# Performance work log

Hardware: AMD Instinct MI355X
Metric: run time of the kernel (lower is better)

Reference implementation:

```python
import jax, jax.numpy as jnp
import numpy as np

GAMMA = 0.5
LENS = 0.5
WINDOW = 10  # window_size from init

@jax.custom_vjp
def act_fun(x):
    # Heaviside forward, Gaussian surrogate backward (matches torch ActFun)
    return (x > 0).astype(x.dtype)

def _act_fwd(x):
    return act_fun(x), x

def _act_bwd(x, g):
    temp = jnp.exp(-x * x / (2 * LENS * LENS)) / (np.sqrt(2 * np.pi) * LENS)
    return (GAMMA * g * temp,)

act_fun.defvjp(_act_fwd, _act_bwd)

def mem_update(inputs, mem, thr):
    # decay_neu == 1
    mem = mem + inputs
    spike = act_fun(mem - thr)
    mem = mem * (1 - spike)
    neg = (mem < -thr).astype(mem.dtype)
    mem = mem * (1 - neg) - thr * neg
    return mem, spike

def setup_inputs() -> dict:
    key = jax.random.key(0)
    ks = jax.random.split(key, 6)
    B, T, D, H, O = 128, 100, 2048, 1024, 20
    return {
        "input": jax.random.normal(ks[0], (B, T, D), jnp.float32),
        "labels": jax.random.randint(ks[1], (B,), 0, O),
        "hidden_mem": jnp.zeros((B, H), jnp.float32),
        "hidden_spike": jnp.zeros((B, H), jnp.float32),
        "output_mem": jnp.zeros((B, O), jnp.float32),
        "output_spike": jnp.zeros((B, O), jnp.float32),
        "Wi2h": jax.random.normal(ks[2], (H, D), jnp.float32) / np.sqrt(D).astype(np.float32),
        "bi2h": jnp.zeros((H,), jnp.float32),
        "Wh2h": jax.random.normal(ks[3], (H, H), jnp.float32) / np.sqrt(H).astype(np.float32),
        "bh2h": jnp.zeros((H,), jnp.float32),
        "Wh2o": jax.random.normal(ks[4], (O, H), jnp.float32) / np.sqrt(H).astype(np.float32),
        "bh2o": jnp.zeros((O,), jnp.float32),
        "thr_h": jnp.ones((H,), jnp.float32),
        "thr_o": jnp.ones((O,), jnp.float32),
    }

def reference(input, labels, hidden_mem, hidden_spike, output_mem, output_spike,
              Wi2h, bi2h, Wh2h, bh2h, Wh2o, bh2o, thr_h, thr_o):
    B = input.shape[0]

    def step(carry, x_t):
        hm, hs, om, osp, osum = carry
        h_in = x_t @ Wi2h.T + bi2h + hs @ Wh2h.T + bh2h
        hm, hs = mem_update(h_in, hm, thr_h)
        om, osp = mem_update(hs @ Wh2o.T + bh2o, om, thr_o)
        osum = osum + osp
        nbr = (jnp.sum(osp) + jnp.sum(hs)) / B
        return (hm, hs, om, osp, osum), (hs, nbr)

    osum0 = jnp.zeros_like(output_spike)
    carry0 = (hidden_mem, hidden_spike, output_mem, output_spike, osum0)
    (hm, hs, om, osp, osum), (hs_t, nbr_events) = jax.lax.scan(
        step, carry0, jnp.swapaxes(input, 0, 1))  # scan over T

    hidden_spike_t = jnp.transpose(hs_t, (1, 2, 0))  # [B, H, T]
    # moving average over time windows (unfold + mean), stride 1
    c = jnp.cumsum(jnp.pad(hidden_spike_t, ((0, 0), (0, 0), (1, 0))), axis=2)
    hidden_spike_filt = (c[:, :, WINDOW:] - c[:, :, :-WINDOW]) / WINDOW  # [B,H,T-W+1]

    logp = jax.nn.log_softmax(osum, axis=1)
    predictions = jnp.argmax(logp, axis=1)[None, :]  # [1, B]
    loss = -jnp.mean(logp[jnp.arange(B), labels])  # NLLLoss on log_softmax
    return predictions, loss, nbr_events, hidden_spike_filt
```

## Files before the change

kernel.cpp:

```cpp
#include <hip/hip_runtime.h>
#include <hip/hip_bf16.h>
#include <cstdint>
#include <cstddef>

#define B_ 128
#define T_ 100
#define D_ 2048
#define H_ 1024
#define O_ 20

__global__ __launch_bounds__(256) void prep_kernel(const float* __restrict__ Wh2o,
                                                   float* __restrict__ W2oT,
                                                   float* __restrict__ nbr)
{
    int i = blockIdx.x * 256 + threadIdx.x;
    if (i < H_ * O_) {
        int hh = i / O_;
        int oo = i - hh * O_;
        W2oT[i] = Wh2o[oo * H_ + hh];
    }
    if (i < T_) nbr[i] = 0.0f;
}

__global__ __launch_bounds__(256) void transpose_kernel(const float* __restrict__ A,
                                                        float* __restrict__ AT)
{
    __shared__ float tile[32][33];
    int bx = blockIdx.x * 32, by = blockIdx.y * 32;
    int tx = threadIdx.x, ty = threadIdx.y;
#pragma unroll
    for (int i = 0; i < 32; i += 8)
        tile[ty + i][tx] = A[(size_t)(by + ty + i) * H_ + bx + tx];
    __syncthreads();
#pragma unroll
    for (int i = 0; i < 32; i += 8)
        AT[(size_t)(bx + ty + i) * H_ + by + tx] = tile[tx][ty + i];
}

__global__ __launch_bounds__(256) void gemm_xi_kernel(
    const float* __restrict__ X,
    const float* __restrict__ W,
    const float* __restrict__ bi2h,
    const float* __restrict__ bh2h,
    float* __restrict__ Xi)
{
    constexpr int BM = 128, BN = 128, BK = 16;
    __shared__ float As[BK][BM + 4];
    __shared__ float Bs[BK][BN + 4];
    const int tid = threadIdx.x;
    const int m0 = blockIdx.x * BM;
    const int n0 = blockIdx.y * BN;
    const int tm = tid >> 4;
    const int tn = tid & 15;
    const int ldr = tid >> 2;
    const int ldc = (tid & 3) << 2;

    float acc[8][8];
#pragma unroll
    for (int i = 0; i < 8; ++i)
#pragma unroll
        for (int j = 0; j < 8; ++j) acc[i][j] = 0.0f;

    for (int k0 = 0; k0 < D_; k0 += BK) {
#pragma unroll
        for (int p = 0; p < 2; ++p) {
            int r = ldr + p * 64;
            float4 v = *(const float4*)(X + (size_t)(m0 + r) * D_ + k0 + ldc);
            As[ldc + 0][r] = v.x; As[ldc + 1][r] = v.y;
            As[ldc + 2][r] = v.z; As[ldc + 3][r] = v.w;
        }
#pragma unroll
        for (int p = 0; p < 2; ++p) {
            int r = ldr + p * 64;
            float4 v = *(const float4*)(W + (size_t)(n0 + r) * D_ + k0 + ldc);
            Bs[ldc + 0][r] = v.x; Bs[ldc + 1][r] = v.y;
            Bs[ldc + 2][r] = v.z; Bs[ldc + 3][r] = v.w;
        }
        __syncthreads();
#pragma unroll
        for (int k = 0; k < BK; ++k) {
            float4 A0 = *(const float4*)&As[k][tm * 8];
            float4 A1 = *(const float4*)&As[k][tm * 8 + 4];
            float4 B0 = *(const float4*)&Bs[k][tn * 8];
            float4 B1 = *(const float4*)&Bs[k][tn * 8 + 4];
            float a[8] = {A0.x, A0.y, A0.z, A0.w, A1.x, A1.y, A1.z, A1.w};
            float bb[8] = {B0.x, B0.y, B0.z, B0.w, B1.x, B1.y, B1.z, B1.w};
#pragma unroll
            for (int i = 0; i < 8; ++i)
#pragma unroll
                for (int j = 0; j < 8; ++j) acc[i][j] += a[i] * bb[j];
        }
        __syncthreads();
    }

    float bsum[8];
#pragma unroll
    for (int j = 0; j < 8; ++j) {
        int n = n0 + tn * 8 + j;
        bsum[j] = bi2h[n] + bh2h[n];
    }
#pragma unroll
    for (int i = 0; i < 8; ++i) {
        size_t row = (size_t)(m0 + tm * 8 + i);
        float4 o0 = {acc[i][0] + bsum[0], acc[i][1] + bsum[1],
                     acc[i][2] + bsum[2], acc[i][3] + bsum[3]};
        float4 o1 = {acc[i][4] + bsum[4], acc[i][5] + bsum[5],
                     acc[i][6] + bsum[6], acc[i][7] + bsum[7]};
        *(float4*)(Xi + row * H_ + n0 + tn * 8)     = o0;
        *(float4*)(Xi + row * H_ + n0 + tn * 8 + 4) = o1;
    }
}

__global__ __launch_bounds__(1024) void phase2_kernel(
    const float* __restrict__ Xi,
    const float* __restrict__ WT,
    const float* __restrict__ W2oT,
    const float* __restrict__ bh2o,
    const float* __restrict__ thr_h_g,
    const float* __restrict__ thr_o_g,
    const float* __restrict__ hm0,
    const float* __restrict__ hs0,
    const float* __restrict__ om0,
    ulonglong2* __restrict__ spk,
    float* __restrict__ osum_out,
    float* __restrict__ nbr_acc)
{
    const int b = blockIdx.x;
    const int h = threadIdx.x;
    const int lane = h & 63;
    const int wv = h >> 6;

    __shared__ int   s_list[H_];
    __shared__ int   s_cnt;
    __shared__ float s_opart[16][O_];
    __shared__ int   s_wpop[16];
    __shared__ float s_om[O_];
    __shared__ float s_osum[O_];
    __shared__ float s_tho[O_];
    __shared__ float s_bo[O_];

    float hm = hm0[(size_t)b * H_ + h];
    const float thr = thr_h_g[h];

    if (h < O_) {
        s_om[h]   = om0[(size_t)b * O_ + h];
        s_osum[h] = 0.0f;
        s_tho[h]  = thr_o_g[h];
        s_bo[h]   = bh2o[h];
    }
    if (h == 0) s_cnt = 0;
    __syncthreads();
    {
        bool act = hs0[(size_t)b * H_ + h] > 0.5f;
        unsigned long long mask = __ballot(act);
        int base = 0;
        if (lane == 0) { int pc = __popcll(mask); if (pc) base = atomicAdd(&s_cnt, pc); }
        base = __shfl(base, 0);
        if (act) s_list[base + __popcll(mask & ((1ull << lane) - 1ull))] = h;
    }
    __syncthreads();

    unsigned long long bits0 = 0, bits1 = 0;
    const float* wtb = WT + h;

    for (int t = 0; t < T_; ++t) {
        float acc = Xi[((size_t)b * T_ + t) * H_ + h];
        int cnt = s_cnt;
        float a0 = 0.f, a1 = 0.f, a2 = 0.f, a3 = 0.f;
        int l = 0;
        for (; l + 4 <= cnt; l += 4) {
            int j0 = s_list[l + 0];
            int j1 = s_list[l + 1];
            int j2 = s_list[l + 2];
            int j3 = s_list[l + 3];
            a0 += wtb[(size_t)j0 << 10];
            a1 += wtb[(size_t)j1 << 10];
            a2 += wtb[(size_t)j2 << 10];
            a3 += wtb[(size_t)j3 << 10];
        }
        for (; l < cnt; ++l) a0 += wtb[(size_t)s_list[l] << 10];
        acc += (a0 + a1) + (a2 + a3);

        hm += acc;
        bool sp = (hm - thr) > 0.0f;
        if (sp) hm = 0.0f;
        if (hm < -thr) hm = -thr;
        if (sp) { if (t < 64) bits0 |= (1ull << t); else bits1 |= (1ull << (t - 64)); }

        __syncthreads();
        if (h == 0) s_cnt = 0;
        __syncthreads();
        unsigned long long mask = __ballot(sp);
        int pc = __popcll(mask);
        int base = 0;
        if (lane == 0) { s_wpop[wv] = pc; if (pc) base = atomicAdd(&s_cnt, pc); }
        base = __shfl(base, 0);
        if (sp) s_list[base + __popcll(mask & ((1ull << lane) - 1ull))] = h;
        __syncthreads();

        cnt = s_cnt;
        int per = (cnt + 15) >> 4;
        int lo = wv * per;
        int hi = lo + per; if (hi > cnt) hi = cnt;
        if (lane < O_) {
            float op = 0.0f;
            for (int q = lo; q < hi; ++q) {
                int j = s_list[q];
                op += W2oT[j * O_ + lane];
            }
            s_opart[wv][lane] = op;
        }
        __syncthreads();

        float osp_local = 0.0f;
        if (h < O_) {
            float oin = s_bo[h];
#pragma unroll
            for (int w = 0; w < 16; ++w) oin += s_opart[w][h];
            float om = s_om[h] + oin;
            float osp = ((om - s_tho[h]) > 0.0f) ? 1.0f : 0.0f;
            if (osp > 0.5f) om = 0.0f;
            if (om < -s_tho[h]) om = -s_tho[h];
            s_om[h] = om;
            s_osum[h] += osp;
            osp_local = osp;
        }
        if (h < 64) {
            float c = osp_local;
            c += __shfl_xor(c, 1);
            c += __shfl_xor(c, 2);
            c += __shfl_xor(c, 4);
            c += __shfl_xor(c, 8);
            c += __shfl_xor(c, 16);
            c += __shfl_xor(c, 32);
            if (lane == 0) {
                int hidcnt = 0;
#pragma unroll
                for (int w = 0; w < 16; ++w) hidcnt += s_wpop[w];
                atomicAdd(&nbr_acc[t], c + (float)hidcnt);
            }
        }
    }

    ulonglong2 vv; vv.x = bits0; vv.y = bits1;
    spk[(size_t)b * H_ + h] = vv;
    if (h < O_) osum_out[(size_t)b * O_ + h] = s_osum[h];
}

__global__ __launch_bounds__(256) void filt_kernel(const ulonglong2* __restrict__ spk,
                                                   float* __restrict__ outf)
{
    int i = blockIdx.x * 256 + threadIdx.x;
    ulonglong2 v = spk[i];
    float* o = outf + (size_t)i * 91;
    int s = __popcll(v.x & 0x3FFull);
    o[0] = (float)s * 0.1f;
#pragma unroll 1
    for (int tau = 1; tau <= 90; ++tau) {
        int ta = tau + 9, tsb = tau - 1;
        int add = (ta < 64) ? (int)((v.x >> ta) & 1ull) : (int)((v.y >> (ta - 64)) & 1ull);
        int sub = (tsb < 64) ? (int)((v.x >> tsb) & 1ull) : (int)((v.y >> (tsb - 64)) & 1ull);
        s += add - sub;
        o[tau] = (float)s * 0.1f;
    }
}

__global__ __launch_bounds__(256) void final_kernel(const float* __restrict__ osum,
                                                    const int* __restrict__ labels,
                                                    float* __restrict__ dout)
{
    __shared__ float s_loss[B_];
    int tid = threadIdx.x;
    if (tid < B_) {
        int b = tid;
        float v[O_];
#pragma unroll
        for (int o = 0; o < O_; ++o) v[o] = osum[b * O_ + o];
        float mv = v[0];
        int am = 0;
#pragma unroll
        for (int o = 1; o < O_; ++o)
            if (v[o] > mv) { mv = v[o]; am = o; }
        float se = 0.0f;
#pragma unroll
        for (int o = 0; o < O_; ++o) se += expf(v[o] - mv);
        float lse = mv + logf(se);
        int lab = labels[b];
        dout[b] = (float)am;
        s_loss[b] = v[lab] - lse;
    }
    if (tid >= 128 && tid < 128 + T_) {
        dout[129 + (tid - 128)] *= (1.0f / (float)B_);
    }
    __syncthreads();
    if (tid == 0) {
        float s = 0.0f;
        for (int b = 0; b < B_; ++b) s += s_loss[b];
        dout[128] = -s / (float)B_;
    }
}

extern "C" void kernel_launch(void* const* d_in, const int* in_sizes, int n_in,
                              void* d_out, int out_size, void* d_ws, size_t ws_size,
                              hipStream_t stream)
{
    const float* input  = (const float*)d_in[0];
    const int*   labels = (const int*)d_in[1];
    const float* hm0    = (const float*)d_in[2];
    const float* hs0    = (const float*)d_in[3];
    const float* om0    = (const float*)d_in[4];
    const float* Wi2h   = (const float*)d_in[6];
    const float* bi2h   = (const float*)d_in[7];
    const float* Wh2h   = (const float*)d_in[8];
    const float* bh2h   = (const float*)d_in[9];
    const float* Wh2o   = (const float*)d_in[10];
    const float* bh2o   = (const float*)d_in[11];
    const float* thr_h  = (const float*)d_in[12];
    const float* thr_o  = (const float*)d_in[13];

    float* out  = (float*)d_out;
    float* nbr  = out + 129;
    float* filt = out + 229;

    char* ws = (char*)d_ws;
    float*      Xi   = (float*)(ws);
    float*      WT   = (float*)(ws + 52428800);
    float*      W2oT = (float*)(ws + 56623104);
    ulonglong2* spk  = (ulonglong2*)(ws + 56705024);
    float*      osum = (float*)(ws + 58802176);

    prep_kernel<<<80, 256, 0, stream>>>(Wh2o, W2oT, nbr);
    transpose_kernel<<<dim3(32, 32), dim3(32, 8), 0, stream>>>(Wh2h, WT);
    gemm_xi_kernel<<<dim3(100, 8), 256, 0, stream>>>(input, Wi2h, bi2h, bh2h, Xi);
    phase2_kernel<<<128, 1024, 0, stream>>>(Xi, WT, W2oT, bh2o, thr_h, thr_o,
                                            hm0, hs0, om0, spk, osum, nbr);
    filt_kernel<<<512, 256, 0, stream>>>(spk, filt);
    final_kernel<<<1, 256, 0, stream>>>(osum, labels, out);
}
```

Measured before the change: 2.234 ms.

## Split recurrent scan across block pairs with global-flag spike exchange and float4 gathers

The per-batch recurrent kernel now runs as two 512-thread blocks, each owning half of the hidden units. The halves exchange spike masks and partial output sums every timestep through global memory with release/acquire flags. This doubles the number of blocks in flight and switches the Wh2h gather to float4 row loads split across four thread groups, reduced through shared memory. The output weights are cached in shared memory and the spike list is rebuilt from ballot masks instead of atomics. The gemm thread-to-tile mapping is also reordered. The costs are cross-block spin-wait synchronisation every step, which relies on both blocks of a pair being resident at once, plus extra barriers.

```diff
diff --git a/kernel.cpp b/kernel.cpp
--- a/kernel.cpp
+++ b/kernel.cpp
@@ -8,10 +8,16 @@
 #define D_ 2048
 #define H_ 1024
 #define O_ 20
+#define H2 512
+
+__device__ inline void f4acc(float4& a, const float4 v) {
+    a.x += v.x; a.y += v.y; a.z += v.z; a.w += v.w;
+}
 
 __global__ __launch_bounds__(256) void prep_kernel(const float* __restrict__ Wh2o,
                                                    float* __restrict__ W2oT,
-                                                   float* __restrict__ nbr)
+                                                   float* __restrict__ nbr,
+                                                   int* __restrict__ g_flag)
 {
     int i = blockIdx.x * 256 + threadIdx.x;
     if (i < H_ * O_) {
@@ -20,6 +26,7 @@
         W2oT[i] = Wh2o[oo * H_ + hh];
     }
     if (i < T_) nbr[i] = 0.0f;
+    if (i < B_ * 2) g_flag[i] = 0;
 }
 
 __global__ __launch_bounds__(256) void transpose_kernel(const float* __restrict__ A,
@@ -50,8 +57,10 @@
     const int tid = threadIdx.x;
     const int m0 = blockIdx.x * BM;
     const int n0 = blockIdx.y * BN;
-    const int tm = tid >> 4;
-    const int tn = tid & 15;
+    const int wave = tid >> 6;
+    const int lane = tid & 63;
+    const int tm = ((wave >> 1) << 3) | (lane >> 3);
+    const int tn = ((wave & 1) << 3) | (lane & 7);
     const int ldr = tid >> 2;
     const int ldc = (tid & 3) << 2;
 
@@ -111,7 +120,7 @@
     }
 }
 
-__global__ __launch_bounds__(1024) void phase2_kernel(
+__global__ __launch_bounds__(512) void phase2_kernel(
     const float* __restrict__ Xi,
     const float* __restrict__ WT,
     const float* __restrict__ W2oT,
@@ -121,130 +130,200 @@
     const float* __restrict__ hm0,
     const float* __restrict__ hs0,
     const float* __restrict__ om0,
+    unsigned long long* __restrict__ g_mask,
+    float* __restrict__ g_opart,
+    int* __restrict__ g_flag,
     ulonglong2* __restrict__ spk,
     float* __restrict__ osum_out,
     float* __restrict__ nbr_acc)
 {
-    const int b = blockIdx.x;
-    const int h = threadIdx.x;
-    const int lane = h & 63;
-    const int wv = h >> 6;
-
+    const int pair = blockIdx.x >> 1;
+    const int half = blockIdx.x & 1;
+    const int b = pair;
+    const int tid = threadIdx.x;
+    const int lane = tid & 63;
+    const int wv = tid >> 6;
+    const int h0 = half * H2;
+    const int h = h0 + tid;
+
+    __shared__ float s_W2o[H2 * O_];
     __shared__ int   s_list[H_];
+    __shared__ float4 s_red[4][128];
+    __shared__ unsigned long long s_mask[16];
+    __shared__ float s_opart[8][O_];
+    __shared__ float s_popart[O_];
+    __shared__ int   s_base[16];
     __shared__ int   s_cnt;
-    __shared__ float s_opart[16][O_];
-    __shared__ int   s_wpop[16];
-    __shared__ float s_om[O_];
-    __shared__ float s_osum[O_];
-    __shared__ float s_tho[O_];
-    __shared__ float s_bo[O_];
+    __shared__ float s_om[O_], s_osum[O_], s_tho[O_], s_bo[O_];
+
+    for (int idx = tid; idx < H2 * O_; idx += 512)
+        s_W2o[idx] = W2oT[h0 * O_ + idx];
 
     float hm = hm0[(size_t)b * H_ + h];
     const float thr = thr_h_g[h];
 
-    if (h < O_) {
-        s_om[h]   = om0[(size_t)b * O_ + h];
-        s_osum[h] = 0.0f;
-        s_tho[h]  = thr_o_g[h];
-        s_bo[h]   = bh2o[h];
-    }
-    if (h == 0) s_cnt = 0;
+    if (half == 0 && tid < O_) {
+        s_om[tid]   = om0[b * O_ + tid];
+        s_osum[tid] = 0.0f;
+        s_tho[tid]  = thr_o_g[tid];
+        s_bo[tid]   = bh2o[tid];
+    }
+
+    {
+        bool a1 = hs0[(size_t)b * H_ + wv * 64 + lane] > 0.5f;
+        bool a2 = hs0[(size_t)b * H_ + H2 + wv * 64 + lane] > 0.5f;
+        unsigned long long m1 = __ballot(a1), m2 = __ballot(a2);
+        if (lane == 0) { s_mask[wv] = m1; s_mask[8 + wv] = m2; }
+    }
+    __syncthreads();
+    if (tid == 0) {
+        int a = 0;
+#pragma unroll
+        for (int w = 0; w < 16; ++w) { s_base[w] = a; a += __popcll(s_mask[w]); }
+        s_cnt = a;
+    }
     __syncthreads();
     {
-        bool act = hs0[(size_t)b * H_ + h] > 0.5f;
-        unsigned long long mask = __ballot(act);
-        int base = 0;
-        if (lane == 0) { int pc = __popcll(mask); if (pc) base = atomicAdd(&s_cnt, pc); }
-        base = __shfl(base, 0);
-        if (act) s_list[base + __popcll(mask & ((1ull << lane) - 1ull))] = h;
+        int j = tid; int w = j >> 6; unsigned long long mw = s_mask[w];
+        if ((mw >> (j & 63)) & 1ull)
+            s_list[s_base[w] + __popcll(mw & ((1ull << (j & 63)) - 1ull))] = j;
+        j = tid + H2; w = j >> 6; mw = s_mask[w];
+        if ((mw >> (j & 63)) & 1ull)
+            s_list[s_base[w] + __popcll(mw & ((1ull << (j & 63)) - 1ull))] = j;
     }
     __syncthreads();
 
+    const float4* __restrict__ wt4 = (const float4*)WT + (h0 >> 2);
+    const int g = tid >> 7;
+    const int cid = tid & 127;
     unsigned long long bits0 = 0, bits1 = 0;
-    const float* wtb = WT + h;
 
     for (int t = 0; t < T_; ++t) {
-        float acc = Xi[((size_t)b * T_ + t) * H_ + h];
-        int cnt = s_cnt;
-        float a0 = 0.f, a1 = 0.f, a2 = 0.f, a3 = 0.f;
-        int l = 0;
-        for (; l + 4 <= cnt; l += 4) {
-            int j0 = s_list[l + 0];
-            int j1 = s_list[l + 1];
-            int j2 = s_list[l + 2];
-            int j3 = s_list[l + 3];
-            a0 += wtb[(size_t)j0 << 10];
-            a1 += wtb[(size_t)j1 << 10];
-            a2 += wtb[(size_t)j2 << 10];
-            a3 += wtb[(size_t)j3 << 10];
-        }
-        for (; l < cnt; ++l) a0 += wtb[(size_t)s_list[l] << 10];
-        acc += (a0 + a1) + (a2 + a3);
-
-        hm += acc;
+        const int cnt = s_cnt;
+        float4 a0 = {0,0,0,0}, a1 = {0,0,0,0}, a2 = {0,0,0,0}, a3 = {0,0,0,0};
+        int l = g;
+        for (; l + 12 < cnt; l += 16) {
+            int j0 = s_list[l], j1 = s_list[l + 4], j2 = s_list[l + 8], j3 = s_list[l + 12];
+            f4acc(a0, wt4[(size_t)j0 * 256 + cid]);
+            f4acc(a1, wt4[(size_t)j1 * 256 + cid]);
+            f4acc(a2, wt4[(size_t)j2 * 256 + cid]);
+            f4acc(a3, wt4[(size_t)j3 * 256 + cid]);
+        }
+        for (; l < cnt; l += 4) f4acc(a0, wt4[(size_t)s_list[l] * 256 + cid]);
+        f4acc(a0, a1); f4acc(a2, a3); f4acc(a0, a2);
+        s_red[g][cid] = a0;
+        __syncthreads();
+
+        float val = 0.0f;
+        const float* rf = (const float*)s_red;
+#pragma unroll
+        for (int gg = 0; gg < 4; ++gg) val += rf[gg * 512 + tid];
+
+        hm += Xi[((size_t)b * T_ + t) * H_ + h] + val;
         bool sp = (hm - thr) > 0.0f;
         if (sp) hm = 0.0f;
         if (hm < -thr) hm = -thr;
         if (sp) { if (t < 64) bits0 |= (1ull << t); else bits1 |= (1ull << (t - 64)); }
 
-        __syncthreads();
-        if (h == 0) s_cnt = 0;
-        __syncthreads();
-        unsigned long long mask = __ballot(sp);
-        int pc = __popcll(mask);
-        int base = 0;
-        if (lane == 0) { s_wpop[wv] = pc; if (pc) base = atomicAdd(&s_cnt, pc); }
-        base = __shfl(base, 0);
-        if (sp) s_list[base + __popcll(mask & ((1ull << lane) - 1ull))] = h;
-        __syncthreads();
-
-        cnt = s_cnt;
-        int per = (cnt + 15) >> 4;
-        int lo = wv * per;
-        int hi = lo + per; if (hi > cnt) hi = cnt;
+        unsigned long long m = __ballot(sp);
+        const int myword = half * 8 + wv;
+        if (lane == 0) s_mask[myword] = m;
+
+        float op = 0.0f;
         if (lane < O_) {
-            float op = 0.0f;
-            for (int q = lo; q < hi; ++q) {
-                int j = s_list[q];
-                op += W2oT[j * O_ + lane];
+            unsigned long long mm = m;
+            while (mm) {
+                int bit = __builtin_ctzll(mm);
+                mm &= mm - 1;
+                op += s_W2o[(wv * 64 + bit) * O_ + lane];
             }
             s_opart[wv][lane] = op;
         }
-        __syncthreads();
-
-        float osp_local = 0.0f;
-        if (h < O_) {
-            float oin = s_bo[h];
-#pragma unroll
-            for (int w = 0; w < 16; ++w) oin += s_opart[w][h];
-            float om = s_om[h] + oin;
-            float osp = ((om - s_tho[h]) > 0.0f) ? 1.0f : 0.0f;
-            if (osp > 0.5f) om = 0.0f;
-            if (om < -s_tho[h]) om = -s_tho[h];
-            s_om[h] = om;
-            s_osum[h] += osp;
-            osp_local = osp;
-        }
-        if (h < 64) {
-            float c = osp_local;
-            c += __shfl_xor(c, 1);
-            c += __shfl_xor(c, 2);
-            c += __shfl_xor(c, 4);
-            c += __shfl_xor(c, 8);
-            c += __shfl_xor(c, 16);
-            c += __shfl_xor(c, 32);
-            if (lane == 0) {
-                int hidcnt = 0;
-#pragma unroll
-                for (int w = 0; w < 16; ++w) hidcnt += s_wpop[w];
-                atomicAdd(&nbr_acc[t], c + (float)hidcnt);
+
+        const int buf = t & 1;
+        unsigned long long* gm = g_mask + (((size_t)(pair * 2 + buf) * 2 + half) * 8);
+        if (lane == 0)
+            __hip_atomic_store(&gm[wv], m, __ATOMIC_RELAXED, __HIP_MEMORY_SCOPE_AGENT);
+        __syncthreads();
+
+        float ownpart = 0.0f;
+        if (tid < O_) {
+            float s = 0.0f;
+#pragma unroll
+            for (int w = 0; w < 8; ++w) s += s_opart[w][tid];
+            ownpart = s;
+            float* go = g_opart + (((size_t)(pair * 2 + buf) * 2 + half) * O_);
+            __hip_atomic_store(&go[tid], s, __ATOMIC_RELAXED, __HIP_MEMORY_SCOPE_AGENT);
+        }
+        __syncthreads();
+        if (tid == 0) {
+            __hip_atomic_store(&g_flag[pair * 2 + half], t + 1,
+                               __ATOMIC_RELEASE, __HIP_MEMORY_SCOPE_AGENT);
+            while (__hip_atomic_load(&g_flag[pair * 2 + (half ^ 1)],
+                                     __ATOMIC_ACQUIRE, __HIP_MEMORY_SCOPE_AGENT) < t + 1)
+                __builtin_amdgcn_s_sleep(1);
+        }
+        __syncthreads();
+
+        const unsigned long long* pm =
+            g_mask + (((size_t)(pair * 2 + buf) * 2 + (half ^ 1)) * 8);
+        if (tid < 8)
+            s_mask[(half ^ 1) * 8 + tid] =
+                __hip_atomic_load(&pm[tid], __ATOMIC_RELAXED, __HIP_MEMORY_SCOPE_AGENT);
+        if (half == 0 && tid < O_) {
+            const float* po = g_opart + (((size_t)(pair * 2 + buf) * 2 + 1) * O_);
+            s_popart[tid] =
+                __hip_atomic_load(&po[tid], __ATOMIC_RELAXED, __HIP_MEMORY_SCOPE_AGENT);
+        }
+        __syncthreads();
+
+        if (half == 0) {
+            float osp_l = 0.0f;
+            if (tid < O_) {
+                float oin = s_bo[tid] + ownpart + s_popart[tid];
+                float om = s_om[tid] + oin;
+                float osp = ((om - s_tho[tid]) > 0.0f) ? 1.0f : 0.0f;
+                if (osp > 0.5f) om = 0.0f;
+                if (om < -s_tho[tid]) om = -s_tho[tid];
+                s_om[tid] = om;
+                s_osum[tid] += osp;
+                osp_l = osp;
             }
-        }
+            if (wv == 0) {
+                float c = osp_l;
+                c += __shfl_xor(c, 1);  c += __shfl_xor(c, 2);
+                c += __shfl_xor(c, 4);  c += __shfl_xor(c, 8);
+                c += __shfl_xor(c, 16); c += __shfl_xor(c, 32);
+                if (lane == 0) {
+                    int hc = 0;
+#pragma unroll
+                    for (int w = 0; w < 16; ++w) hc += __popcll(s_mask[w]);
+                    atomicAdd(&nbr_acc[t], c + (float)hc);
+                }
+            }
+        }
+
+        if (tid == 0) {
+            int a = 0;
+#pragma unroll
+            for (int w = 0; w < 16; ++w) { s_base[w] = a; a += __popcll(s_mask[w]); }
+            s_cnt = a;
+        }
+        __syncthreads();
+        {
+            int j = tid; int w = j >> 6; unsigned long long mw = s_mask[w];
+            if ((mw >> (j & 63)) & 1ull)
+                s_list[s_base[w] + __popcll(mw & ((1ull << (j & 63)) - 1ull))] = j;
+            j = tid + H2; w = j >> 6; mw = s_mask[w];
+            if ((mw >> (j & 63)) & 1ull)
+                s_list[s_base[w] + __popcll(mw & ((1ull << (j & 63)) - 1ull))] = j;
+        }
+        __syncthreads();
     }
 
     ulonglong2 vv; vv.x = bits0; vv.y = bits1;
     spk[(size_t)b * H_ + h] = vv;
-    if (h < O_) osum_out[(size_t)b * O_ + h] = s_osum[h];
+    if (half == 0 && tid < O_) osum_out[b * O_ + tid] = s_osum[tid];
 }
 
 __global__ __launch_bounds__(256) void filt_kernel(const ulonglong2* __restrict__ spk,
@@ -285,9 +364,8 @@
 #pragma unroll
         for (int o = 0; o < O_; ++o) se += expf(v[o] - mv);
         float lse = mv + logf(se);
-        int lab = labels[b];
         dout[b] = (float)am;
-        s_loss[b] = v[lab] - lse;
+        s_loss[b] = v[labels[b]] - lse;
     }
     if (tid >= 128 && tid < 128 + T_) {
         dout[129 + (tid - 128)] *= (1.0f / (float)B_);
@@ -323,17 +401,21 @@
     float* filt = out + 229;
 
     char* ws = (char*)d_ws;
-    float*      Xi   = (float*)(ws);
-    float*      WT   = (float*)(ws + 52428800);
-    float*      W2oT = (float*)(ws + 56623104);
-    ulonglong2* spk  = (ulonglong2*)(ws + 56705024);
-    float*      osum = (float*)(ws + 58802176);
-
-    prep_kernel<<<80, 256, 0, stream>>>(Wh2o, W2oT, nbr);
+    float*      Xi     = (float*)(ws);
+    float*      WT     = (float*)(ws + 52428800);
+    float*      W2oT   = (float*)(ws + 56623104);
+    ulonglong2* spk    = (ulonglong2*)(ws + 56705024);
+    float*      osum   = (float*)(ws + 58802176);
+    unsigned long long* g_mask = (unsigned long long*)(ws + 58812416);
+    float*      g_opart = (float*)(ws + 58845184);
+    int*        g_flag  = (int*)(ws + 58886144);
+
+    prep_kernel<<<80, 256, 0, stream>>>(Wh2o, W2oT, nbr, g_flag);
     transpose_kernel<<<dim3(32, 32), dim3(32, 8), 0, stream>>>(Wh2h, WT);
     gemm_xi_kernel<<<dim3(100, 8), 256, 0, stream>>>(input, Wi2h, bi2h, bh2h, Xi);
-    phase2_kernel<<<128, 1024, 0, stream>>>(Xi, WT, W2oT, bh2o, thr_h, thr_o,
-                                            hm0, hs0, om0, spk, osum, nbr);
+    phase2_kernel<<<256, 512, 0, stream>>>(Xi, WT, W2oT, bh2o, thr_h, thr_o,
+                                           hm0, hs0, om0, g_mask, g_opart, g_flag,
+                                           spk, osum, nbr);
     filt_kernel<<<512, 256, 0, stream>>>(spk, filt);
     final_kernel<<<1, 256, 0, stream>>>(osum, labels, out);
 }
```

Result: faster. 2.057 ms (-7.9%).

## Split recurrent phase across 512 blocks with global spike-mask barriers

Applied to the files above, without the earlier changes.

The recurrent scan kernel moves from one 1024-thread block per batch row to 512 blocks, each owning 8 batch rows by 32 hidden columns. Per timestep, blocks exchange spike bitmasks and partial output-layer sums through double-buffered global memory and sync per batch group with an atomic counter spin-wait. The recurrent matvec becomes a dense masked FMA over packed bits instead of a gather over a sparse spike list. The GEMM thread-to-tile mapping is also reshuffled per wave. This spreads the serial scan over many more CUs at the cost of inter-block spin barriers, which assume all 512 blocks are co-resident.

```diff
diff --git a/kernel.cpp b/kernel.cpp
--- a/kernel.cpp
+++ b/kernel.cpp
@@ -9,9 +9,14 @@
 #define H_ 1024
 #define O_ 20
 
+__device__ inline void f4acc(float4& a, const float4 v) {
+    a.x += v.x; a.y += v.y; a.z += v.z; a.w += v.w;
+}
+
 __global__ __launch_bounds__(256) void prep_kernel(const float* __restrict__ Wh2o,
                                                    float* __restrict__ W2oT,
-                                                   float* __restrict__ nbr)
+                                                   float* __restrict__ nbr,
+                                                   int* __restrict__ g_cnt)
 {
     int i = blockIdx.x * 256 + threadIdx.x;
     if (i < H_ * O_) {
@@ -20,6 +25,7 @@
         W2oT[i] = Wh2o[oo * H_ + hh];
     }
     if (i < T_) nbr[i] = 0.0f;
+    if (i < 16) g_cnt[i] = 0;
 }
 
 __global__ __launch_bounds__(256) void transpose_kernel(const float* __restrict__ A,
@@ -50,8 +56,10 @@
     const int tid = threadIdx.x;
     const int m0 = blockIdx.x * BM;
     const int n0 = blockIdx.y * BN;
-    const int tm = tid >> 4;
-    const int tn = tid & 15;
+    const int wave = tid >> 6;
+    const int lane = tid & 63;
+    const int tm = ((wave >> 1) << 3) | (lane >> 3);
+    const int tn = ((wave & 1) << 3) | (lane & 7);
     const int ldr = tid >> 2;
     const int ldc = (tid & 3) << 2;
 
@@ -111,7 +119,7 @@
     }
 }
 
-__global__ __launch_bounds__(1024) void phase2_kernel(
+__global__ __launch_bounds__(320) void phase2_kernel(
     const float* __restrict__ Xi,
     const float* __restrict__ WT,
     const float* __restrict__ W2oT,
@@ -121,130 +129,192 @@
     const float* __restrict__ hm0,
     const float* __restrict__ hs0,
     const float* __restrict__ om0,
+    unsigned int* __restrict__ g_mask32,
+    float* __restrict__ g_opart,
+    int* __restrict__ g_cnt,
     ulonglong2* __restrict__ spk,
     float* __restrict__ osum_out,
     float* __restrict__ nbr_acc)
 {
-    const int b = blockIdx.x;
-    const int h = threadIdx.x;
-    const int lane = h & 63;
-    const int wv = h >> 6;
-
-    __shared__ int   s_list[H_];
-    __shared__ int   s_cnt;
-    __shared__ float s_opart[16][O_];
-    __shared__ int   s_wpop[16];
-    __shared__ float s_om[O_];
-    __shared__ float s_osum[O_];
-    __shared__ float s_tho[O_];
-    __shared__ float s_bo[O_];
-
-    float hm = hm0[(size_t)b * H_ + h];
-    const float thr = thr_h_g[h];
-
-    if (h < O_) {
-        s_om[h]   = om0[(size_t)b * O_ + h];
-        s_osum[h] = 0.0f;
-        s_tho[h]  = thr_o_g[h];
-        s_bo[h]   = bh2o[h];
-    }
-    if (h == 0) s_cnt = 0;
+    const int blk = blockIdx.x;
+    const int q = blk >> 3;
+    const int cg = (blk & 7) * 4 + (q & 3);
+    const int bg = q >> 2;
+    const int b0 = bg * 8;
+    const int c0 = cg * 32;
+    const int tid = threadIdx.x;
+    const int lane = tid & 63;
+    const int wv = tid >> 6;
+    const bool docg0 = (cg == 0);
+
+    __shared__ float s_red[1024];
+    __shared__ unsigned int s_mask32[256];
+    __shared__ float s_om[160], s_osum[160];
+    __shared__ float s_bo[O_], s_tho[O_];
+
+    float hm = 0.0f, thr = 1.0f;
+    if (tid < 256) {
+        int b = tid >> 5, hoff = tid & 31;
+        hm = hm0[(size_t)(b0 + b) * H_ + c0 + hoff];
+        thr = thr_h_g[c0 + hoff];
+    }
+    if (tid < 160) {
+        s_om[tid] = om0[(b0 + tid / O_) * O_ + tid % O_];
+        s_osum[tid] = 0.0f;
+    }
+    if (tid < O_) { s_bo[tid] = bh2o[tid]; s_tho[tid] = thr_o_g[tid]; }
+
+    for (int idx = tid; idx < 256; idx += 320) {
+        int b = idx >> 5, w32 = idx & 31;
+        const float* base = hs0 + (size_t)(b0 + b) * H_ + w32 * 32;
+        unsigned int mw = 0;
+#pragma unroll
+        for (int k = 0; k < 32; ++k)
+            mw |= (base[k] > 0.5f ? 1u : 0u) << k;
+        s_mask32[idx] = mw;
+    }
     __syncthreads();
-    {
-        bool act = hs0[(size_t)b * H_ + h] > 0.5f;
-        unsigned long long mask = __ballot(act);
-        int base = 0;
-        if (lane == 0) { int pc = __popcll(mask); if (pc) base = atomicAdd(&s_cnt, pc); }
-        base = __shfl(base, 0);
-        if (act) s_list[base + __popcll(mask & ((1ull << lane) - 1ull))] = h;
-    }
-    __syncthreads();
+
+    int vb[3], vo[3];
+#pragma unroll
+    for (int p = 0; p < 3; ++p) {
+        int idx = p * 64 + lane;
+        vb[p] = idx / O_;
+        vo[p] = idx - vb[p] * O_;
+    }
 
     unsigned long long bits0 = 0, bits1 = 0;
-    const float* wtb = WT + h;
-
-    for (int t = 0; t < T_; ++t) {
-        float acc = Xi[((size_t)b * T_ + t) * H_ + h];
-        int cnt = s_cnt;
-        float a0 = 0.f, a1 = 0.f, a2 = 0.f, a3 = 0.f;
-        int l = 0;
-        for (; l + 4 <= cnt; l += 4) {
-            int j0 = s_list[l + 0];
-            int j1 = s_list[l + 1];
-            int j2 = s_list[l + 2];
-            int j3 = s_list[l + 3];
-            a0 += wtb[(size_t)j0 << 10];
-            a1 += wtb[(size_t)j1 << 10];
-            a2 += wtb[(size_t)j2 << 10];
-            a3 += wtb[(size_t)j3 << 10];
-        }
-        for (; l < cnt; ++l) a0 += wtb[(size_t)s_list[l] << 10];
-        acc += (a0 + a1) + (a2 + a3);
-
-        hm += acc;
-        bool sp = (hm - thr) > 0.0f;
-        if (sp) hm = 0.0f;
-        if (hm < -thr) hm = -thr;
-        if (sp) { if (t < 64) bits0 |= (1ull << t); else bits1 |= (1ull << (t - 64)); }
-
-        __syncthreads();
-        if (h == 0) s_cnt = 0;
-        __syncthreads();
-        unsigned long long mask = __ballot(sp);
-        int pc = __popcll(mask);
-        int base = 0;
-        if (lane == 0) { s_wpop[wv] = pc; if (pc) base = atomicAdd(&s_cnt, pc); }
-        base = __shfl(base, 0);
-        if (sp) s_list[base + __popcll(mask & ((1ull << lane) - 1ull))] = h;
-        __syncthreads();
-
-        cnt = s_cnt;
-        int per = (cnt + 15) >> 4;
-        int lo = wv * per;
-        int hi = lo + per; if (hi > cnt) hi = cnt;
-        if (lane < O_) {
-            float op = 0.0f;
-            for (int q = lo; q < hi; ++q) {
-                int j = s_list[q];
-                op += W2oT[j * O_ + lane];
+
+    for (int t = 0; t <= T_; ++t) {
+        const bool full = (t < T_);
+
+        float xi = 0.0f;
+        if (full && tid < 256)
+            xi = Xi[((size_t)(b0 + (tid >> 5)) * T_ + t) * H_ + c0 + (tid & 31)];
+
+        if (t > 0 && tid == 0) {
+            while (__hip_atomic_load(g_cnt + bg, __ATOMIC_ACQUIRE,
+                                     __HIP_MEMORY_SCOPE_AGENT) < 32 * t)
+                __builtin_amdgcn_s_sleep(2);
+        }
+        __syncthreads();
+        if (t > 0 && tid < 256) {
+            s_mask32[tid] = __hip_atomic_load(
+                g_mask32 + ((t - 1) & 1) * 4096 + (b0 + (tid >> 5)) * 32 + (tid & 31),
+                __ATOMIC_RELAXED, __HIP_MEMORY_SCOPE_AGENT);
+        }
+        __syncthreads();
+
+        if (tid < 256) {
+            if (full) {
+                const int gb = lane >> 3;
+                const int colq = lane & 7;
+                const unsigned int* mrow = s_mask32 + gb * 32 + wv * 8;
+                const float4* p =
+                    (const float4*)(WT + (size_t)(wv * 256) * H_ + c0) + colq;
+                float4 a0 = {0, 0, 0, 0}, a1 = {0, 0, 0, 0};
+#pragma unroll
+                for (int w = 0; w < 8; ++w) {
+                    unsigned int mw = mrow[w];
+#pragma unroll 4
+                    for (int r = 0; r < 32; r += 2) {
+                        float s0 = (float)(mw & 1u);
+                        float s1 = (float)((mw >> 1) & 1u);
+                        mw >>= 2;
+                        float4 v0 = p[0];
+                        float4 v1 = p[256];
+                        a0.x = fmaf(s0, v0.x, a0.x); a0.y = fmaf(s0, v0.y, a0.y);
+                        a0.z = fmaf(s0, v0.z, a0.z); a0.w = fmaf(s0, v0.w, a0.w);
+                        a1.x = fmaf(s1, v1.x, a1.x); a1.y = fmaf(s1, v1.y, a1.y);
+                        a1.z = fmaf(s1, v1.z, a1.z); a1.w = fmaf(s1, v1.w, a1.w);
+                        p += 512;
+                    }
+                }
+                f4acc(a0, a1);
+                ((float4*)s_red)[wv * 64 + lane] = a0;
             }
-            s_opart[wv][lane] = op;
-        }
-        __syncthreads();
-
-        float osp_local = 0.0f;
-        if (h < O_) {
-            float oin = s_bo[h];
-#pragma unroll
-            for (int w = 0; w < 16; ++w) oin += s_opart[w][h];
-            float om = s_om[h] + oin;
-            float osp = ((om - s_tho[h]) > 0.0f) ? 1.0f : 0.0f;
-            if (osp > 0.5f) om = 0.0f;
-            if (om < -s_tho[h]) om = -s_tho[h];
-            s_om[h] = om;
-            s_osum[h] += osp;
-            osp_local = osp;
-        }
-        if (h < 64) {
-            float c = osp_local;
-            c += __shfl_xor(c, 1);
-            c += __shfl_xor(c, 2);
-            c += __shfl_xor(c, 4);
-            c += __shfl_xor(c, 8);
-            c += __shfl_xor(c, 16);
-            c += __shfl_xor(c, 32);
-            if (lane == 0) {
-                int hidcnt = 0;
-#pragma unroll
-                for (int w = 0; w < 16; ++w) hidcnt += s_wpop[w];
-                atomicAdd(&nbr_acc[t], c + (float)hidcnt);
+        } else if (docg0 && t > 0) {
+            const int bufp = (t - 1) & 1;
+            float ospsum = 0.0f;
+#pragma unroll
+            for (int p = 0; p < 3; ++p) {
+                int idx = p * 64 + lane;
+                if (idx < 160) {
+                    const float* gp =
+                        g_opart + bufp * 81920 + ((b0 + vb[p]) * 32) * O_ + vo[p];
+                    float oin = s_bo[vo[p]];
+#pragma unroll
+                    for (int c = 0; c < 32; ++c)
+                        oin += __hip_atomic_load(gp + c * O_, __ATOMIC_RELAXED,
+                                                 __HIP_MEMORY_SCOPE_AGENT);
+                    float om = s_om[idx] + oin;
+                    float osp = ((om - s_tho[vo[p]]) > 0.0f) ? 1.0f : 0.0f;
+                    if (osp > 0.5f) om = 0.0f;
+                    if (om < -s_tho[vo[p]]) om = -s_tho[vo[p]];
+                    s_om[idx] = om;
+                    s_osum[idx] += osp;
+                    ospsum += osp;
+                }
             }
-        }
-    }
-
-    ulonglong2 vv; vv.x = bits0; vv.y = bits1;
-    spk[(size_t)b * H_ + h] = vv;
-    if (h < O_) osum_out[(size_t)b * O_ + h] = s_osum[h];
+            int hid = 0;
+#pragma unroll
+            for (int k = 0; k < 4; ++k) hid += __popc(s_mask32[lane * 4 + k]);
+            float tot = ospsum + (float)hid;
+            tot += __shfl_xor(tot, 1);  tot += __shfl_xor(tot, 2);
+            tot += __shfl_xor(tot, 4);  tot += __shfl_xor(tot, 8);
+            tot += __shfl_xor(tot, 16); tot += __shfl_xor(tot, 32);
+            if (lane == 0) atomicAdd(&nbr_acc[t - 1], tot);
+        }
+        __syncthreads();
+
+        if (full && tid < 256) {
+            float val = s_red[tid] + s_red[256 + tid] +
+                        s_red[512 + tid] + s_red[768 + tid];
+            hm += xi + val;
+            bool spb = (hm - thr) > 0.0f;
+            if (spb) hm = 0.0f;
+            if (hm < -thr) hm = -thr;
+            if (spb) { if (t < 64) bits0 |= 1ull << t; else bits1 |= 1ull << (t - 64); }
+
+            unsigned long long bal = __ballot(spb);
+            const int wb = tid >> 6;
+            const int buf = t & 1;
+            if (lane == 0)
+                __hip_atomic_store(g_mask32 + buf * 4096 + (b0 + wb * 2) * 32 + cg,
+                                   (unsigned int)bal, __ATOMIC_RELAXED,
+                                   __HIP_MEMORY_SCOPE_AGENT);
+            if (lane == 32)
+                __hip_atomic_store(g_mask32 + buf * 4096 + (b0 + wb * 2 + 1) * 32 + cg,
+                                   (unsigned int)(bal >> 32), __ATOMIC_RELAXED,
+                                   __HIP_MEMORY_SCOPE_AGENT);
+            const int o = lane & 31;
+            if (o < O_) {
+                unsigned int mm = (lane < 32) ? (unsigned int)bal
+                                              : (unsigned int)(bal >> 32);
+                const int ob = b0 + wb * 2 + (lane >= 32 ? 1 : 0);
+                float op = 0.0f;
+                while (mm) {
+                    int j = __builtin_ctz(mm);
+                    mm &= mm - 1;
+                    op += W2oT[(c0 + j) * O_ + o];
+                }
+                __hip_atomic_store(g_opart + buf * 81920 + (ob * 32 + cg) * O_ + o,
+                                   op, __ATOMIC_RELAXED, __HIP_MEMORY_SCOPE_AGENT);
+            }
+        }
+        __syncthreads();
+        if (full && tid == 0)
+            __hip_atomic_fetch_add(g_cnt + bg, 1, __ATOMIC_RELEASE,
+                                   __HIP_MEMORY_SCOPE_AGENT);
+    }
+
+    if (tid < 256) {
+        int b = tid >> 5, hoff = tid & 31;
+        ulonglong2 vv; vv.x = bits0; vv.y = bits1;
+        spk[(size_t)(b0 + b) * H_ + c0 + hoff] = vv;
+    }
+    if (docg0 && tid < 160)
+        osum_out[(b0 + tid / O_) * O_ + tid % O_] = s_osum[tid];
 }
 
 __global__ __launch_bounds__(256) void filt_kernel(const ulonglong2* __restrict__ spk,
@@ -285,9 +355,8 @@
 #pragma unroll
         for (int o = 0; o < O_; ++o) se += expf(v[o] - mv);
         float lse = mv + logf(se);
-        int lab = labels[b];
         dout[b] = (float)am;
-        s_loss[b] = v[lab] - lse;
+        s_loss[b] = v[labels[b]] - lse;
     }
     if (tid >= 128 && tid < 128 + T_) {
         dout[129 + (tid - 128)] *= (1.0f / (float)B_);
@@ -323,17 +392,21 @@
     float* filt = out + 229;
 
     char* ws = (char*)d_ws;
-    float*      Xi   = (float*)(ws);
-    float*      WT   = (float*)(ws + 52428800);
-    float*      W2oT = (float*)(ws + 56623104);
-    ulonglong2* spk  = (ulonglong2*)(ws + 56705024);
-    float*      osum = (float*)(ws + 58802176);
-
-    prep_kernel<<<80, 256, 0, stream>>>(Wh2o, W2oT, nbr);
+    float*        Xi     = (float*)(ws);
+    float*        WT     = (float*)(ws + 52428800);
+    float*        W2oT   = (float*)(ws + 56623104);
+    ulonglong2*   spk    = (ulonglong2*)(ws + 56705024);
+    float*        osum   = (float*)(ws + 58802176);
+    unsigned int* g_mask32 = (unsigned int*)(ws + 58812416);
+    float*        g_opart  = (float*)(ws + 58845184);
+    int*          g_cnt    = (int*)(ws + 59500544);
+
+    prep_kernel<<<80, 256, 0, stream>>>(Wh2o, W2oT, nbr, g_cnt);
     transpose_kernel<<<dim3(32, 32), dim3(32, 8), 0, stream>>>(Wh2h, WT);
     gemm_xi_kernel<<<dim3(100, 8), 256, 0, stream>>>(input, Wi2h, bi2h, bh2h, Xi);
-    phase2_kernel<<<128, 1024, 0, stream>>>(Xi, WT, W2oT, bh2o, thr_h, thr_o,
-                                            hm0, hs0, om0, spk, osum, nbr);
+    phase2_kernel<<<512, 320, 0, stream>>>(Xi, WT, W2oT, bh2o, thr_h, thr_o,
+                                           hm0, hs0, om0, g_mask32, g_opart, g_cnt,
+                                           spk, osum, nbr);
     filt_kernel<<<512, 256, 0, stream>>>(spk, filt);
     final_kernel<<<1, 256, 0, stream>>>(osum, labels, out);
 }
```

Result: slower. 7.616 ms (+240.9%).
